# Kernel tuning notes

Measured on AMD Instinct MI355X. Metric: run time of the kernel, lower is better.

The kernel has to match this reference:

```python
import jax, jax.numpy as jnp
import numpy as np

RATIO = 0.5  # init arg: fraction of channels kept by topk


def setup_inputs() -> dict:
    key = jax.random.key(0)
    x = jax.random.normal(key, (32, 512, 64, 64), dtype=jnp.float32)
    # Fixed curvature stencil from the original module (nn.Parameter with constant init)
    weight = jnp.array(
        [[[[-1.0 / 16, 5.0 / 16, -1.0 / 16],
           [5.0 / 16, -1.0, 5.0 / 16],
           [-1.0 / 16, 5.0 / 16, -1.0 / 16]]]], dtype=jnp.float32)
    return {"x": x, "weight": weight}


def reference(x, weight):
    B, C, H, W = x.shape
    k = int(RATIO * C)
    # Depthwise-style conv: treat each (b, c) plane as its own sample with 1 channel.
    xr = x.reshape(B * C, 1, H, W)
    # torch F.conv2d is cross-correlation with VALID padding; lax conv matches (no kernel flip).
    out = jax.lax.conv_general_dilated(
        xr, weight, window_strides=(1, 1), padding='VALID',
        dimension_numbers=('NCHW', 'OIHW', 'NCHW'))  # [B*C, 1, H-2, W-2]
    # Curvature score per channel: sum of |response| over spatial dims.
    p = jnp.abs(out).sum(axis=(-1, -2)).reshape(B, C)  # [B, C]
    _, idx = jax.lax.top_k(p, k)  # [B, k]
    # Batched channel gather (replaces the per-sample Python loop + index_select).
    selected = jnp.take_along_axis(x, idx[:, :, None, None], axis=1)  # [B, k, H, W]
    return selected
```

## Files before the change

### kernel.cpp

```cpp
#include <hip/hip_runtime.h>

#define HW     64
#define PLANE  4096
#define OW     62
#define NCH    512
#define NB     32
#define TOPK   256

__global__ __launch_bounds__(256) void score_kernel(const float* __restrict__ x,
                                                    double* __restrict__ p) {
    __shared__ float tile[PLANE];
    const int plane = blockIdx.x;
    const int tid = threadIdx.x;

    const float4* src4 = (const float4*)(x + (size_t)plane * PLANE);
    float4* dst4 = (float4*)tile;
    #pragma unroll
    for (int i = 0; i < PLANE / 4 / 256; ++i)
        dst4[tid + 256 * i] = src4[tid + 256 * i];
    __syncthreads();

    double acc = 0.0;
    if (tid < 248) {
        const int r = tid >> 2;
        const int s = tid & 3;
        const int c0 = s * 16;

        float f0[20], f1[20], f2[20];
        const float* row0 = tile + r * HW + c0;
        const float* row1 = row0 + HW;
        const float* row2 = row0 + 2 * HW;
        #pragma unroll
        for (int v = 0; v < 4; ++v) {
            *(float4*)(f0 + 4 * v) = *(const float4*)(row0 + 4 * v);
            *(float4*)(f1 + 4 * v) = *(const float4*)(row1 + 4 * v);
            *(float4*)(f2 + 4 * v) = *(const float4*)(row2 + 4 * v);
        }
        if (s < 3) {
            *(float4*)(f0 + 16) = *(const float4*)(row0 + 16);
            *(float4*)(f1 + 16) = *(const float4*)(row1 + 16);
            *(float4*)(f2 + 16) = *(const float4*)(row2 + 16);
        } else {
            #pragma unroll
            for (int j = 16; j < 20; ++j) { f0[j] = 0.f; f1[j] = 0.f; f2[j] = 0.f; }
        }

        const int nvalid = (s == 3) ? 14 : 16;
        const double C5 = 0.3125;
        const double CM = -0.0625;

        #pragma unroll
        for (int u = 0; u < 16; ++u) {
            double a0 = (double)f0[u]     + (double)f2[u];
            double a1 = (double)f0[u + 1] + (double)f2[u + 1];
            double a2 = (double)f0[u + 2] + (double)f2[u + 2];
            double plus = a1 + (double)f1[u] + (double)f1[u + 2];
            double diag = a0 + a2;
            double resp = fma(C5, plus, fma(CM, diag, -(double)f1[u + 1]));
            acc += (u < nvalid) ? fabs(resp) : 0.0;
        }
    }

    #pragma unroll
    for (int off = 32; off > 0; off >>= 1)
        acc += __shfl_down(acc, off, 64);

    __shared__ double wsum[4];
    const int wave = tid >> 6;
    if ((tid & 63) == 0) wsum[wave] = acc;
    __syncthreads();
    if (tid == 0)
        p[plane] = wsum[0] + wsum[1] + wsum[2] + wsum[3];
}

__global__ __launch_bounds__(512) void topk_kernel(const double* __restrict__ p,
                                                   int* __restrict__ idx) {
    __shared__ double sp[NCH];
    const int b = blockIdx.x;
    const int c = threadIdx.x;
    sp[c] = p[(size_t)b * NCH + c];
    __syncthreads();

    const double mine = sp[c];
    int rank = 0;
    for (int j = 0; j < NCH; ++j) {
        const double v = sp[j];
        rank += (v > mine) || (v == mine && j < c) ? 1 : 0;
    }
    if (rank < TOPK)
        idx[(size_t)b * TOPK + rank] = c;
}

__global__ __launch_bounds__(256) void gather_kernel(const float* __restrict__ x,
                                                     const int* __restrict__ idx,
                                                     float* __restrict__ out) {
    const int bj = blockIdx.x;
    const int b = bj >> 8;
    const int ch = idx[bj];
    const float4* src = (const float4*)(x + ((size_t)b * NCH + ch) * PLANE);
    float4* dst = (float4*)(out + (size_t)bj * PLANE);
    const int tid = threadIdx.x;
    #pragma unroll
    for (int i = 0; i < 4; ++i)
        dst[tid + 256 * i] = src[tid + 256 * i];
}

extern "C" void kernel_launch(void* const* d_in, const int* in_sizes, int n_in,
                              void* d_out, int out_size, void* d_ws, size_t ws_size,
                              hipStream_t stream) {
    const float* x = (const float*)d_in[0];
    float* out = (float*)d_out;

    double* p = (double*)d_ws;
    int* idx = (int*)((char*)d_ws + (size_t)NB * NCH * sizeof(double));

    score_kernel<<<NB * NCH, 256, 0, stream>>>(x, p);
    topk_kernel<<<NB, NCH, 0, stream>>>(p, idx);
    gather_kernel<<<NB * TOPK, 256, 0, stream>>>(x, idx, out);
}
```

Measured before the change: 435.8 us.

## Pad score tile, compute stencil in fp32, reverse gather order with nontemporal stores

The stencil response is now computed in fp32 instead of fp64, and only the absolute values are accumulated in double. The shared tile gets a padded row stride of 68 floats to reduce LDS bank conflicts on the three-row loads. The gather kernel walks blocks in reverse order so it can reuse planes still in cache from the score pass, and it writes with nontemporal stores. The fp32 stencil can change tie or near-tie ordering in top-k relative to the fp64 version.

```diff
diff --git a/kernel.cpp b/kernel.cpp
--- a/kernel.cpp
+++ b/kernel.cpp
@@ -6,18 +6,24 @@
 #define NCH    512
 #define NB     32
 #define TOPK   256
+#define LSTR   68
+
+typedef float floatx4 __attribute__((ext_vector_type(4)));
 
 __global__ __launch_bounds__(256) void score_kernel(const float* __restrict__ x,
                                                     double* __restrict__ p) {
-    __shared__ float tile[PLANE];
+    __shared__ float tile[64 * LSTR];
     const int plane = blockIdx.x;
     const int tid = threadIdx.x;
 
     const float4* src4 = (const float4*)(x + (size_t)plane * PLANE);
-    float4* dst4 = (float4*)tile;
     #pragma unroll
-    for (int i = 0; i < PLANE / 4 / 256; ++i)
-        dst4[tid + 256 * i] = src4[tid + 256 * i];
+    for (int i = 0; i < 4; ++i) {
+        const int g = tid + 256 * i;
+        const int row = g >> 4;
+        const int c4 = g & 15;
+        *(float4*)(tile + row * LSTR + c4 * 4) = src4[g];
+    }
     __syncthreads();
 
     double acc = 0.0;
@@ -27,9 +33,9 @@
         const int c0 = s * 16;
 
         float f0[20], f1[20], f2[20];
-        const float* row0 = tile + r * HW + c0;
-        const float* row1 = row0 + HW;
-        const float* row2 = row0 + 2 * HW;
+        const float* row0 = tile + r * LSTR + c0;
+        const float* row1 = row0 + LSTR;
+        const float* row2 = row0 + 2 * LSTR;
         #pragma unroll
         for (int v = 0; v < 4; ++v) {
             *(float4*)(f0 + 4 * v) = *(const float4*)(row0 + 4 * v);
@@ -46,18 +52,18 @@
         }
 
         const int nvalid = (s == 3) ? 14 : 16;
-        const double C5 = 0.3125;
-        const double CM = -0.0625;
+        const float C5 = 0.3125f;
+        const float CM = -0.0625f;
 
         #pragma unroll
         for (int u = 0; u < 16; ++u) {
-            double a0 = (double)f0[u]     + (double)f2[u];
-            double a1 = (double)f0[u + 1] + (double)f2[u + 1];
-            double a2 = (double)f0[u + 2] + (double)f2[u + 2];
-            double plus = a1 + (double)f1[u] + (double)f1[u + 2];
-            double diag = a0 + a2;
-            double resp = fma(C5, plus, fma(CM, diag, -(double)f1[u + 1]));
-            acc += (u < nvalid) ? fabs(resp) : 0.0;
+            float a0 = f0[u]     + f2[u];
+            float a1 = f0[u + 1] + f2[u + 1];
+            float a2 = f0[u + 2] + f2[u + 2];
+            float plus = a1 + f1[u] + f1[u + 2];
+            float diag = a0 + a2;
+            float resp = fmaf(C5, plus, fmaf(CM, diag, -f1[u + 1]));
+            acc += (u < nvalid) ? (double)fabsf(resp) : 0.0;
         }
     }
 
@@ -94,15 +100,17 @@
 __global__ __launch_bounds__(256) void gather_kernel(const float* __restrict__ x,
                                                      const int* __restrict__ idx,
                                                      float* __restrict__ out) {
-    const int bj = blockIdx.x;
+    const int bj = NB * TOPK - 1 - blockIdx.x;
     const int b = bj >> 8;
     const int ch = idx[bj];
-    const float4* src = (const float4*)(x + ((size_t)b * NCH + ch) * PLANE);
-    float4* dst = (float4*)(out + (size_t)bj * PLANE);
+    const floatx4* src = (const floatx4*)(x + ((size_t)b * NCH + ch) * PLANE);
+    floatx4* dst = (floatx4*)(out + (size_t)bj * PLANE);
     const int tid = threadIdx.x;
     #pragma unroll
-    for (int i = 0; i < 4; ++i)
-        dst[tid + 256 * i] = src[tid + 256 * i];
+    for (int i = 0; i < 4; ++i) {
+        floatx4 v = src[tid + 256 * i];
+        __builtin_nontemporal_store(v, dst + tid + 256 * i);
+    }
 }
 
 extern "C" void kernel_launch(void* const* d_in, const int* in_sizes, int n_in,
```

New measurement: 419.0 us. -3.8%, faster.
